# Performance work log

Measured on AMD Instinct MI355X. Metric: run time of the kernel, lower is better.

Reference implementation:

```python
import jax, jax.numpy as jnp
import numpy as np

B, SX, SY, C, M, OUT = 1024, 180, 130, 3, 16, 180
VR_MEAN, VR_STD, EPS = 400.0, 100.0, 1e-5
FLAT = C * SX * SY  # 70200
HID1, HID2 = 2808, OUT


def setup_inputs() -> dict:
    key = jax.random.key(0)
    ks = jax.random.split(key, 16)
    scale = 1.0 / (C * C)
    inp = {
        "x": jax.random.normal(ks[0], (B, SX, SY + 1), dtype=jnp.float32),
        # spectral weights stored as real pairs [in,out,m1,m2,2] like torch view_as_real
        "w1_0": scale * jax.random.uniform(ks[1], (C, C, M, M, 2), dtype=jnp.float32),
        "w2_0": scale * jax.random.uniform(ks[2], (C, C, M, M, 2), dtype=jnp.float32),
        "w1_1": scale * jax.random.uniform(ks[3], (C, C, M, M, 2), dtype=jnp.float32),
        "w2_1": scale * jax.random.uniform(ks[4], (C, C, M, M, 2), dtype=jnp.float32),
        "out1_w1": jax.random.normal(ks[5], (HID1, FLAT), dtype=jnp.float32) * (1.0 / np.sqrt(FLAT)),
        "out1_b1": jnp.zeros((HID1,), dtype=jnp.float32),
        "out1_w2": jax.random.normal(ks[6], (OUT, HID1), dtype=jnp.float32) * (1.0 / np.sqrt(HID1)),
        "out1_b2": jnp.zeros((OUT,), dtype=jnp.float32),
        "reg2_w1": jax.random.normal(ks[7], (OUT, 2 * OUT), dtype=jnp.float32) * (1.0 / np.sqrt(2 * OUT)),
        "reg2_b1": jnp.zeros((OUT,), dtype=jnp.float32),
        "reg2_w2": jax.random.normal(ks[8], (OUT, OUT), dtype=jnp.float32) * (1.0 / np.sqrt(OUT)),
        "reg2_b2": jnp.zeros((OUT,), dtype=jnp.float32),
    }
    return inp


def _cplx(w):
    return w[..., 0] + 1j * w[..., 1]


def _inorm(x):
    # InstanceNorm2d, affine=False: normalize each (b,c) map over spatial dims
    mu = jnp.mean(x, axis=(2, 3), keepdims=True)
    var = jnp.var(x, axis=(2, 3), keepdims=True)
    return (x - mu) * jax.lax.rsqrt(var + EPS)


def _spectral_conv(x, w1, w2):
    # x: [B,C,SX,SY]
    xft = jnp.fft.rfft2(x)  # [B,C,SX,SY//2+1]
    o1 = jnp.einsum('bixy,ioxy->boxy', xft[:, :, :M, :M], _cplx(w1))
    o2 = jnp.einsum('bixy,ioxy->boxy', xft[:, :, -M:, :M], _cplx(w2))
    out_ft = jnp.zeros(xft.shape, dtype=xft.dtype)
    out_ft = out_ft.at[:, :, :M, :M].set(o1)
    out_ft = out_ft.at[:, :, -M:, :M].set(o2)
    return jnp.fft.irfft2(out_ft, s=(SX, SY))


def reference(x, w1_0, w2_0, w1_1, w2_1, out1_w1, out1_b1, out1_w2, out1_b2,
              reg2_w1, reg2_b1, reg2_w2, reg2_b2):
    x0 = x[:, :, -1]                      # [B,180]
    h = x[:, :SX, :-1][..., None]         # [B,180,130,1]
    gx = jnp.linspace(0.0, 1.0, SX, dtype=jnp.float32)[None, :, None, None]
    gy = jnp.linspace(0.0, 1.0, SY, dtype=jnp.float32)[None, None, :, None]
    grid = jnp.concatenate([jnp.broadcast_to(gx, (x.shape[0], SX, SY, 1)),
                            jnp.broadcast_to(gy, (x.shape[0], SX, SY, 1))], axis=-1)
    h = jnp.concatenate([h, grid], axis=-1)          # [B,180,130,3]
    h = jnp.transpose(h, (0, 3, 1, 2))               # [B,3,180,130]
    h = jax.nn.gelu(_inorm(_spectral_conv(_inorm(h), w1_0, w2_0)), approximate=False)
    h = jax.nn.gelu(_inorm(_spectral_conv(_inorm(h), w1_1, w2_1)), approximate=False)
    h = h.reshape(h.shape[0], -1)                    # [B,70200]
    h = jax.nn.relu(h @ out1_w1.T + out1_b1) @ out1_w2.T + out1_b2  # [B,180]
    x0n = (x0 - VR_MEAN) / VR_STD
    # stack pred & normalized residual per output, interleave: [B,180,2] -> [B,360]
    h = jnp.stack([h, x0n], axis=-1).reshape(h.shape[0], -1)
    h = jax.nn.relu(h @ reg2_w1.T + reg2_b1) @ reg2_w2.T + reg2_b2
    return h * VR_STD + VR_MEAN
```

## Files before the change

kernel.cpp:

```cpp
#include <hip/hip_runtime.h>
#include <hip/hip_bf16.h>
#include <math.h>

#ifndef M_PI
#define M_PI 3.14159265358979323846
#endif

#define B_    1024
#define SX    180
#define SY    130
#define NC    3
#define IMG   23400
#define FLATK 70200
#define KPAD  70208
#define HID1  2808
#define NOUT  180
#define XROW  131
#define H1STR 2816
#define KSTEPS 2194
#define KCH8   275
#define NKZ    8

typedef __attribute__((ext_vector_type(8))) short short8;
typedef __attribute__((ext_vector_type(4))) float f32x4;
typedef __attribute__((address_space(3))) unsigned int lds_u32;
typedef __attribute__((address_space(1))) const unsigned int glb_u32;

#define TY_SH   5632
#define TX_SH   12800
#define TXI_SH  13824
#define TIY_SH  6144

__device__ __forceinline__ unsigned short f2bf(float f){
  __hip_bfloat16 h = __float2bfloat16(f);
  return __builtin_bit_cast(unsigned short, h);
}
__device__ __forceinline__ float bf2f(unsigned short u){
  __hip_bfloat16 h = __builtin_bit_cast(__hip_bfloat16, u);
  return __bfloat162float(h);
}
__device__ __forceinline__ void split_bf(float f, unsigned short &hi, unsigned short &lo){
  hi = f2bf(f);
  lo = f2bf(f - bf2f(hi));
}
__device__ __forceinline__ void gl_lds16(const void* g, void* l){
  __builtin_amdgcn_global_load_lds((glb_u32*)g, (lds_u32*)l, 16, 0, 0);
}
__device__ __forceinline__ float gelu_f(float v){
  return 0.5f * v * (1.0f + erff(v * 0.70710678118654752f));
}
__device__ __forceinline__ short8 ld_g8(const unsigned short* p){
  return *(const short8*)p;
}

__global__ void k_tables2(unsigned short* __restrict__ TyH, unsigned short* __restrict__ TyL,
                          unsigned short* __restrict__ TxH, unsigned short* __restrict__ TxL,
                          unsigned short* __restrict__ TxiH, unsigned short* __restrict__ TxiL,
                          unsigned short* __restrict__ TiyH, unsigned short* __restrict__ TiyL){
  int i = blockIdx.x*256 + threadIdx.x;
  unsigned short h, l;
  if (i < TY_SH){
    int m = i/168, y = i%168;
    float v = 0.f;
    if (m < 32 && y < SY){
      int ky = m>>1, ri = m&1;
      double ang = 2.0*M_PI*(double)((ky*y)%SY)/(double)SY;
      v = ri ? (float)(-sin(ang)) : (float)cos(ang);
    }
    split_bf(v,h,l); TyH[i]=h; TyL[i]=l;
  }
  if (i < TX_SH){
    int n = i/200, x = i%200;
    float v = 0.f;
    if (x < SX){
      int kxi = n>>1, ri = n&1;
      int kx = (kxi<16)? kxi : kxi+148;
      double ang = 2.0*M_PI*(double)((kx*x)%SX)/(double)SX;
      v = ri ? (float)sin(ang) : (float)cos(ang);
    }
    split_bf(v,h,l); TxH[i]=h; TxL[i]=l;
  }
  if (i < TXI_SH){
    int x = i/72, k = i%72;
    float v = 0.f;
    if (x < SX && k < 64){
      int kxi = k>>1, ri = k&1;
      int kx = (kxi<16)? kxi : kxi+148;
      double ang = 2.0*M_PI*(double)((kx*x)%SX)/(double)SX;
      v = (float)((ri ? sin(ang) : cos(ang)) / (double)SX);
    }
    split_bf(v,h,l); TxiH[i]=h; TxiL[i]=l;
  }
  if (i < TIY_SH){
    int y = i/40, m = i%40;
    float v = 0.f;
    if (y < SY && m < 32){
      int ky = m>>1, ri = m&1;
      if (m == 0) v = 1.0f/(float)SY;
      else if (m == 1) v = 0.f;
      else {
        double ang = 2.0*M_PI*(double)((ky*y)%SY)/(double)SY;
        v = (float)((ri ? -2.0*sin(ang) : 2.0*cos(ang)) / (double)SY);
      }
    }
    split_bf(v,h,l); TiyH[i]=h; TiyL[i]=l;
  }
}

__global__ __launch_bounds__(256) void k_fwd0(const float* __restrict__ xin,
                                              const unsigned short* __restrict__ TyH,
                                              const unsigned short* __restrict__ TyL,
                                              const unsigned short* __restrict__ TxH,
                                              const unsigned short* __restrict__ TxL,
                                              float* __restrict__ U1,
                                              float* __restrict__ Ug){
  constexpr int DHI = 0;
  constexpr int YTH = 0, YTL = 6400;
  __shared__ unsigned short LB[32256];
  __shared__ float sred[2][4];
  __shared__ float mb[2];
  int t = threadIdx.x, lane = t&63, wv = t>>6, lr = lane&15, lq = lane>>4;
  int bid = blockIdx.x;

  float s = 0.f, ss = 0.f;
  for (int i=t; i<7680; i+=256){
    int row = i/40, c4 = (i - row*40)*4;
    float v[4];
    #pragma unroll
    for (int j=0;j<4;j++){
      int y = c4 + j;
      float val = 0.f;
      if (row < SX && y < SY){
        if (bid < B_)       val = xin[(size_t)bid*(SX*XROW) + row*XROW + y];
        else if (bid == B_) val = (float)row * (1.0f/179.0f);
        else                val = (float)y * (1.0f/129.0f);
      }
      s += val; ss += val*val;
      v[j] = val;
    }
    ushort4 u; u.x=f2bf(v[0]); u.y=f2bf(v[1]); u.z=f2bf(v[2]); u.w=f2bf(v[3]);
    *(ushort4*)&LB[DHI + row*168 + c4] = u;
  }
  for (int o = 32; o >= 1; o >>= 1){ s += __shfl_down(s,o); ss += __shfl_down(ss,o); }
  if (lane == 0){ sred[0][wv] = s; sred[1][wv] = ss; }
  __syncthreads();
  if (t == 0){
    float S = sred[0][0]+sred[0][1]+sred[0][2]+sred[0][3];
    float SS = sred[1][0]+sred[1][1]+sred[1][2]+sred[1][3];
    float mean = S * (1.0f/IMG);
    float var  = SS * (1.0f/IMG) - mean*mean;
    mb[0] = mean; mb[1] = rsqrtf(var + 1e-5f);
  }
  __syncthreads();

  f32x4 acc[2][3] = {};
  #pragma unroll
  for (int ks=0; ks<5; ks++){
    short8 tyh[2], tyl[2];
    #pragma unroll
    for (int mt=0; mt<2; mt++){
      tyh[mt] = ld_g8(&TyH[(mt*16+lr)*168 + ks*32 + lq*8]);
      tyl[mt] = ld_g8(&TyL[(mt*16+lr)*168 + ks*32 + lq*8]);
    }
    #pragma unroll
    for (int j=0; j<3; j++){
      int xr = (wv*3 + j)*16 + lr;
      short8 dh = *(const short8*)&LB[DHI + xr*168 + ks*32 + lq*8];
      #pragma unroll
      for (int mt=0; mt<2; mt++){
        acc[mt][j] = __builtin_amdgcn_mfma_f32_16x16x32_bf16(tyh[mt], dh, acc[mt][j], 0,0,0);
        acc[mt][j] = __builtin_amdgcn_mfma_f32_16x16x32_bf16(tyl[mt], dh, acc[mt][j], 0,0,0);
      }
    }
  }
  __syncthreads();

  {
    float mean = mb[0], istd = mb[1];
    #pragma unroll
    for (int mt=0; mt<2; mt++){
      #pragma unroll
      for (int j=0; j<3; j++){
        int xr = (wv*3 + j)*16 + lr;
        #pragma unroll
        for (int r=0; r<4; r++){
          int m = mt*16 + lq*4 + r;
          float v = acc[mt][j][r];
          if (m == 0) v -= 130.0f*mean;
          v *= istd;
          unsigned short h,l; split_bf(v,h,l);
          LB[YTH + m*200 + xr] = h;
          LB[YTL + m*200 + xr] = l;
        }
      }
    }
  }
  __syncthreads();

  f32x4 acc2[2] = {};
  #pragma unroll
  for (int ks=0; ks<6; ks++){
    short8 txh = ld_g8(&TxH[(wv*16+lr)*200 + ks*32 + lq*8]);
    short8 txl = ld_g8(&TxL[(wv*16+lr)*200 + ks*32 + lq*8]);
    #pragma unroll
    for (int mt=0; mt<2; mt++){
      short8 yh = *(const short8*)&LB[YTH + (mt*16+lr)*200 + ks*32 + lq*8];
      short8 yl = *(const short8*)&LB[YTL + (mt*16+lr)*200 + ks*32 + lq*8];
      acc2[mt] = __builtin_amdgcn_mfma_f32_16x16x32_bf16(yh, txh, acc2[mt], 0,0,0);
      acc2[mt] = __builtin_amdgcn_mfma_f32_16x16x32_bf16(yl, txh, acc2[mt], 0,0,0);
      acc2[mt] = __builtin_amdgcn_mfma_f32_16x16x32_bf16(yh, txl, acc2[mt], 0,0,0);
    }
  }
  float* Ub = (bid < B_) ? (U1 + (size_t)bid*2048) : (Ug + (size_t)(bid - B_)*2048);
  #pragma unroll
  for (int mt=0; mt<2; mt++){
    #pragma unroll
    for (int r=0; r<4; r++){
      int m = mt*16 + lq*4 + r;
      int n = wv*16 + lr;
      Ub[m*64 + n] = acc2[mt][r];
    }
  }
}

__global__ __launch_bounds__(256) void k_mid(const float* __restrict__ U1,
                                             const float* __restrict__ Ug,
                                             const float* __restrict__ w1,
                                             const float* __restrict__ w2,
                                             const unsigned short* __restrict__ TxiH,
                                             const unsigned short* __restrict__ TxiL,
                                             const unsigned short* __restrict__ TiyH,
                                             const unsigned short* __restrict__ TiyL,
                                             const unsigned short* __restrict__ TyH,
                                             const unsigned short* __restrict__ TyL,
                                             const unsigned short* __restrict__ TxH,
                                             const unsigned short* __restrict__ TxL,
                                             float* __restrict__ U2){
  constexpr int ZFH = 0, ZFL = 2304, GH = 4608, GL = 12288;
  constexpr int DAT = 0;
  constexpr int YTH = 0, YTL = 6400;
  __shared__ unsigned short LB[32256];
  __shared__ float sred[2][4];
  __shared__ float mb[2];
  int t = threadIdx.x, lane = t&63, wv = t>>6, lr = lane&15, lq = lane>>4;
  int bid = blockIdx.x, b = bid/3, o = bid - b*3;

  #pragma unroll
  for (int pp=0; pp<2; pp++){
    int p = t + pp*256;
    int kxi = p & 31, ky = p >> 5;
    const float* w = (kxi < 16) ? w1 : w2;
    int kxm = kxi & 15;
    float ar = 0.f, ai = 0.f;
    #pragma unroll
    for (int i=0; i<3; i++){
      const float* Ui = (i==0) ? (U1 + (size_t)b*2048) : (Ug + (size_t)(i-1)*2048);
      float P = Ui[(2*ky  )*64 + 2*kxi  ];
      float Q = Ui[(2*ky  )*64 + 2*kxi+1];
      float R = Ui[(2*ky+1)*64 + 2*kxi  ];
      float S = Ui[(2*ky+1)*64 + 2*kxi+1];
      float zr = P + S, zi = R - Q;
      size_t wo = ((((size_t)i*3 + o)*16 + kxm)*16 + ky)*2;
      float wr = w[wo], wi = w[wo+1];
      ar += zr*wr - zi*wi;
      ai += zr*wi + zi*wr;
    }
    unsigned short hr,lr_, hi,li, hn,ln;
    split_bf(ar,hr,lr_); split_bf(ai,hi,li); split_bf(-ai,hn,ln);
    LB[ZFH + (2*ky  )*72 + 2*kxi  ] = hr;  LB[ZFL + (2*ky  )*72 + 2*kxi  ] = lr_;
    LB[ZFH + (2*ky  )*72 + 2*kxi+1] = hn;  LB[ZFL + (2*ky  )*72 + 2*kxi+1] = ln;
    LB[ZFH + (2*ky+1)*72 + 2*kxi  ] = hi;  LB[ZFL + (2*ky+1)*72 + 2*kxi  ] = li;
    LB[ZFH + (2*ky+1)*72 + 2*kxi+1] = hr;  LB[ZFL + (2*ky+1)*72 + 2*kxi+1] = lr_;
  }
  __syncthreads();

  f32x4 acc1[2][3] = {};
  #pragma unroll
  for (int ks=0; ks<2; ks++){
    short8 zh[2], zl[2];
    #pragma unroll
    for (int mt=0; mt<2; mt++){
      zh[mt] = *(const short8*)&LB[ZFH + (mt*16+lr)*72 + ks*32 + lq*8];
      zl[mt] = *(const short8*)&LB[ZFL + (mt*16+lr)*72 + ks*32 + lq*8];
    }
    #pragma unroll
    for (int j=0; j<3; j++){
      int x = (wv*3 + j)*16 + lr;
      short8 txh = ld_g8(&TxiH[x*72 + ks*32 + lq*8]);
      short8 txl = ld_g8(&TxiL[x*72 + ks*32 + lq*8]);
      #pragma unroll
      for (int mt=0; mt<2; mt++){
        acc1[mt][j] = __builtin_amdgcn_mfma_f32_16x16x32_bf16(zh[mt], txh, acc1[mt][j], 0,0,0);
        acc1[mt][j] = __builtin_amdgcn_mfma_f32_16x16x32_bf16(zl[mt], txh, acc1[mt][j], 0,0,0);
        acc1[mt][j] = __builtin_amdgcn_mfma_f32_16x16x32_bf16(zh[mt], txl, acc1[mt][j], 0,0,0);
      }
    }
  }
  #pragma unroll
  for (int mt=0; mt<2; mt++){
    #pragma unroll
    for (int j=0; j<3; j++){
      int x = (wv*3 + j)*16 + lr;
      #pragma unroll
      for (int r=0; r<4; r++){
        int m = mt*16 + lq*4 + r;
        unsigned short h,l; split_bf(acc1[mt][j][r], h, l);
        LB[GH + x*40 + m] = h;
        LB[GL + x*40 + m] = l;
      }
    }
  }
  __syncthreads();

  f32x4 acc2[3][9] = {};
  #pragma unroll
  for (int i=0; i<3; i++){
    int x = (wv*3 + i)*16 + lr;
    short8 gh = *(const short8*)&LB[GH + x*40 + lq*8];
    short8 gl = *(const short8*)&LB[GL + x*40 + lq*8];
    #pragma unroll
    for (int yt=0; yt<9; yt++){
      short8 tyh = ld_g8(&TiyH[(yt*16+lr)*40 + lq*8]);
      short8 tyl = ld_g8(&TiyL[(yt*16+lr)*40 + lq*8]);
      acc2[i][yt] = __builtin_amdgcn_mfma_f32_16x16x32_bf16(gh, tyh, acc2[i][yt], 0,0,0);
      acc2[i][yt] = __builtin_amdgcn_mfma_f32_16x16x32_bf16(gl, tyh, acc2[i][yt], 0,0,0);
      acc2[i][yt] = __builtin_amdgcn_mfma_f32_16x16x32_bf16(gh, tyl, acc2[i][yt], 0,0,0);
    }
  }

  float s = 0.f, ss = 0.f;
  #pragma unroll
  for (int i=0; i<3; i++){
    int xt = wv*3 + i;
    #pragma unroll
    for (int yt=0; yt<9; yt++){
      #pragma unroll
      for (int r=0; r<4; r++){
        int x = xt*16 + lq*4 + r;
        int y = yt*16 + lr;
        if (x < SX && y < SY){
          float v = acc2[i][yt][r];
          s += v; ss += v*v;
        }
      }
    }
  }
  for (int off = 32; off >= 1; off >>= 1){ s += __shfl_down(s,off); ss += __shfl_down(ss,off); }
  if (lane == 0){ sred[0][wv] = s; sred[1][wv] = ss; }
  __syncthreads();
  if (t == 0){
    float S = sred[0][0]+sred[0][1]+sred[0][2]+sred[0][3];
    float SS = sred[1][0]+sred[1][1]+sred[1][2]+sred[1][3];
    float mean = S * (1.0f/IMG);
    float var  = SS * (1.0f/IMG) - mean*mean;
    mb[0] = mean; mb[1] = rsqrtf(var + 1e-5f);
  }
  __syncthreads();
  float mean1 = mb[0], istd1 = mb[1];

  for (int i=t; i<8064; i+=256)
    *(ushort4*)&LB[DAT + i*4] = make_ushort4(0,0,0,0);
  float s2 = 0.f, ss2 = 0.f;
  #pragma unroll
  for (int i=0; i<3; i++){
    int xt = wv*3 + i;
    #pragma unroll
    for (int yt=0; yt<9; yt++){
      #pragma unroll
      for (int r=0; r<4; r++){
        int x = xt*16 + lq*4 + r;
        int y = yt*16 + lr;
        float d = 0.f;
        if (x < SX && y < SY){
          d = gelu_f((acc2[i][yt][r] - mean1) * istd1);
          s2 += d; ss2 += d*d;
        }
        acc2[i][yt][r] = d;
      }
    }
  }
  for (int off = 32; off >= 1; off >>= 1){ s2 += __shfl_down(s2,off); ss2 += __shfl_down(ss2,off); }
  if (lane == 0){ sred[0][wv] = s2; sred[1][wv] = ss2; }
  __syncthreads();
  if (t == 0){
    float S = sred[0][0]+sred[0][1]+sred[0][2]+sred[0][3];
    float SS = sred[1][0]+sred[1][1]+sred[1][2]+sred[1][3];
    float mean = S * (1.0f/IMG);
    float var  = SS * (1.0f/IMG) - mean*mean;
    mb[0] = mean; mb[1] = rsqrtf(var + 1e-5f);
  }
  __syncthreads();

  #pragma unroll
  for (int i=0; i<3; i++){
    int xt = wv*3 + i;
    #pragma unroll
    for (int yt=0; yt<9; yt++){
      #pragma unroll
      for (int r=0; r<4; r++){
        int x = xt*16 + lq*4 + r;
        int y = yt*16 + lr;
        if (x < SX && y < SY)
          LB[DAT + x*168 + y] = f2bf(acc2[i][yt][r]);
      }
    }
  }
  __syncthreads();

  f32x4 accf[2][3] = {};
  #pragma unroll
  for (int ks=0; ks<5; ks++){
    short8 tyh[2], tyl[2];
    #pragma unroll
    for (int mt=0; mt<2; mt++){
      tyh[mt] = ld_g8(&TyH[(mt*16+lr)*168 + ks*32 + lq*8]);
      tyl[mt] = ld_g8(&TyL[(mt*16+lr)*168 + ks*32 + lq*8]);
    }
    #pragma unroll
    for (int j=0; j<3; j++){
      int xr = (wv*3 + j)*16 + lr;
      short8 dh = *(const short8*)&LB[DAT + xr*168 + ks*32 + lq*8];
      #pragma unroll
      for (int mt=0; mt<2; mt++){
        accf[mt][j] = __builtin_amdgcn_mfma_f32_16x16x32_bf16(tyh[mt], dh, accf[mt][j], 0,0,0);
        accf[mt][j] = __builtin_amdgcn_mfma_f32_16x16x32_bf16(tyl[mt], dh, accf[mt][j], 0,0,0);
      }
    }
  }
  __syncthreads();

  {
    float mean2 = mb[0], istd2 = mb[1];
    #pragma unroll
    for (int mt=0; mt<2; mt++){
      #pragma unroll
      for (int j=0; j<3; j++){
        int xr = (wv*3 + j)*16 + lr;
        #pragma unroll
        for (int r=0; r<4; r++){
          int m = mt*16 + lq*4 + r;
          float v = accf[mt][j][r];
          if (m == 0) v -= 130.0f*mean2;
          v *= istd2;
          unsigned short h,l; split_bf(v,h,l);
          LB[YTH + m*200 + xr] = h;
          LB[YTL + m*200 + xr] = l;
        }
      }
    }
  }
  __syncthreads();

  f32x4 accu[2] = {};
  #pragma unroll
  for (int ks=0; ks<6; ks++){
    short8 txh = ld_g8(&TxH[(wv*16+lr)*200 + ks*32 + lq*8]);
    short8 txl = ld_g8(&TxL[(wv*16+lr)*200 + ks*32 + lq*8]);
    #pragma unroll
    for (int mt=0; mt<2; mt++){
      short8 yh = *(const short8*)&LB[YTH + (mt*16+lr)*200 + ks*32 + lq*8];
      short8 yl = *(const short8*)&LB[YTL + (mt*16+lr)*200 + ks*32 + lq*8];
      accu[mt] = __builtin_amdgcn_mfma_f32_16x16x32_bf16(yh, txh, accu[mt], 0,0,0);
      accu[mt] = __builtin_amdgcn_mfma_f32_16x16x32_bf16(yl, txh, accu[mt], 0,0,0);
      accu[mt] = __builtin_amdgcn_mfma_f32_16x16x32_bf16(yh, txl, accu[mt], 0,0,0);
    }
  }
  float* Ub = U2 + (size_t)bid*2048;
  #pragma unroll
  for (int mt=0; mt<2; mt++){
    #pragma unroll
    for (int r=0; r<4; r++){
      int m = mt*16 + lq*4 + r;
      int n = wv*16 + lr;
      Ub[m*64 + n] = accu[mt][r];
    }
  }
}

__global__ __launch_bounds__(256) void k_inv1(const float* __restrict__ U2,
                                              const float* __restrict__ w1,
                                              const float* __restrict__ w2,
                                              const unsigned short* __restrict__ TxiH,
                                              const unsigned short* __restrict__ TxiL,
                                              const unsigned short* __restrict__ TiyH,
                                              const unsigned short* __restrict__ TiyL,
                                              unsigned short* __restrict__ Abf){
  constexpr int ZFH = 0, ZFL = 2304, GH = 4608, GL = 12288;
  __shared__ unsigned short LB[19968];
  __shared__ float sred[2][4];
  __shared__ float mb[2];
  int t = threadIdx.x, lane = t&63, wv = t>>6, lr = lane&15, lq = lane>>4;
  int bid = blockIdx.x, b = bid/3, o = bid - b*3;

  #pragma unroll
  for (int pp=0; pp<2; pp++){
    int p = t + pp*256;
    int kxi = p & 31, ky = p >> 5;
    const float* w = (kxi < 16) ? w1 : w2;
    int kxm = kxi & 15;
    float ar = 0.f, ai = 0.f;
    #pragma unroll
    for (int i=0; i<3; i++){
      const float* Ui = U2 + ((size_t)b*3 + i)*2048;
      float P = Ui[(2*ky  )*64 + 2*kxi  ];
      float Q = Ui[(2*ky  )*64 + 2*kxi+1];
      float R = Ui[(2*ky+1)*64 + 2*kxi  ];
      float S = Ui[(2*ky+1)*64 + 2*kxi+1];
      float zr = P + S, zi = R - Q;
      size_t wo = ((((size_t)i*3 + o)*16 + kxm)*16 + ky)*2;
      float wr = w[wo], wi = w[wo+1];
      ar += zr*wr - zi*wi;
      ai += zr*wi + zi*wr;
    }
    unsigned short hr,lr_, hi,li, hn,ln;
    split_bf(ar,hr,lr_); split_bf(ai,hi,li); split_bf(-ai,hn,ln);
    LB[ZFH + (2*ky  )*72 + 2*kxi  ] = hr;  LB[ZFL + (2*ky  )*72 + 2*kxi  ] = lr_;
    LB[ZFH + (2*ky  )*72 + 2*kxi+1] = hn;  LB[ZFL + (2*ky  )*72 + 2*kxi+1] = ln;
    LB[ZFH + (2*ky+1)*72 + 2*kxi  ] = hi;  LB[ZFL + (2*ky+1)*72 + 2*kxi  ] = li;
    LB[ZFH + (2*ky+1)*72 + 2*kxi+1] = hr;  LB[ZFL + (2*ky+1)*72 + 2*kxi+1] = lr_;
  }
  __syncthreads();

  f32x4 acc1[2][3] = {};
  #pragma unroll
  for (int ks=0; ks<2; ks++){
    short8 zh[2], zl[2];
    #pragma unroll
    for (int mt=0; mt<2; mt++){
      zh[mt] = *(const short8*)&LB[ZFH + (mt*16+lr)*72 + ks*32 + lq*8];
      zl[mt] = *(const short8*)&LB[ZFL + (mt*16+lr)*72 + ks*32 + lq*8];
    }
    #pragma unroll
    for (int j=0; j<3; j++){
      int x = (wv*3 + j)*16 + lr;
      short8 txh = ld_g8(&TxiH[x*72 + ks*32 + lq*8]);
      short8 txl = ld_g8(&TxiL[x*72 + ks*32 + lq*8]);
      #pragma unroll
      for (int mt=0; mt<2; mt++){
        acc1[mt][j] = __builtin_amdgcn_mfma_f32_16x16x32_bf16(zh[mt], txh, acc1[mt][j], 0,0,0);
        acc1[mt][j] = __builtin_amdgcn_mfma_f32_16x16x32_bf16(zl[mt], txh, acc1[mt][j], 0,0,0);
        acc1[mt][j] = __builtin_amdgcn_mfma_f32_16x16x32_bf16(zh[mt], txl, acc1[mt][j], 0,0,0);
      }
    }
  }
  #pragma unroll
  for (int mt=0; mt<2; mt++){
    #pragma unroll
    for (int j=0; j<3; j++){
      int x = (wv*3 + j)*16 + lr;
      #pragma unroll
      for (int r=0; r<4; r++){
        int m = mt*16 + lq*4 + r;
        unsigned short h,l; split_bf(acc1[mt][j][r], h, l);
        LB[GH + x*40 + m] = h;
        LB[GL + x*40 + m] = l;
      }
    }
  }
  __syncthreads();

  f32x4 acc2[3][9] = {};
  #pragma unroll
  for (int i=0; i<3; i++){
    int x = (wv*3 + i)*16 + lr;
    short8 gh = *(const short8*)&LB[GH + x*40 + lq*8];
    short8 gl = *(const short8*)&LB[GL + x*40 + lq*8];
    #pragma unroll
    for (int yt=0; yt<9; yt++){
      short8 tyh = ld_g8(&TiyH[(yt*16+lr)*40 + lq*8]);
      short8 tyl = ld_g8(&TiyL[(yt*16+lr)*40 + lq*8]);
      acc2[i][yt] = __builtin_amdgcn_mfma_f32_16x16x32_bf16(gh, tyh, acc2[i][yt], 0,0,0);
      acc2[i][yt] = __builtin_amdgcn_mfma_f32_16x16x32_bf16(gl, tyh, acc2[i][yt], 0,0,0);
      acc2[i][yt] = __builtin_amdgcn_mfma_f32_16x16x32_bf16(gh, tyl, acc2[i][yt], 0,0,0);
    }
  }

  float s = 0.f, ss = 0.f;
  #pragma unroll
  for (int i=0; i<3; i++){
    int xt = wv*3 + i;
    #pragma unroll
    for (int yt=0; yt<9; yt++){
      #pragma unroll
      for (int r=0; r<4; r++){
        int x = xt*16 + lq*4 + r;
        int y = yt*16 + lr;
        if (x < SX && y < SY){
          float v = acc2[i][yt][r];
          s += v; ss += v*v;
        }
      }
    }
  }
  for (int off = 32; off >= 1; off >>= 1){ s += __shfl_down(s,off); ss += __shfl_down(ss,off); }
  if (lane == 0){ sred[0][wv] = s; sred[1][wv] = ss; }
  __syncthreads();
  if (t == 0){
    float S = sred[0][0]+sred[0][1]+sred[0][2]+sred[0][3];
    float SS = sred[1][0]+sred[1][1]+sred[1][2]+sred[1][3];
    float mean = S * (1.0f/IMG);
    float var  = SS * (1.0f/IMG) - mean*mean;
    mb[0] = mean; mb[1] = rsqrtf(var + 1e-5f);
  }
  __syncthreads();
  float mean = mb[0], istd = mb[1];

  unsigned short* dst = Abf + (size_t)b*KPAD + (size_t)o*IMG;
  #pragma unroll
  for (int i=0; i<3; i++){
    int xt = wv*3 + i;
    #pragma unroll
    for (int yt=0; yt<9; yt++){
      #pragma unroll
      for (int r=0; r<4; r++){
        int x = xt*16 + lq*4 + r;
        int y = yt*16 + lr;
        if (x < SX && y < SY){
          float v = (acc2[i][yt][r] - mean) * istd;
          dst[x*SY + y] = f2bf(gelu_f(v));
        }
      }
    }
  }
}

__global__ void k_cvt_w(const float* __restrict__ W, unsigned short* __restrict__ Wbf){
  int row = blockIdx.y;
  int gi = blockIdx.x*256 + threadIdx.x;
  if (gi >= KPAD/8) return;
  unsigned short* dst = Wbf + (size_t)row*KPAD + gi*8;
  if (gi*8 >= FLATK){
    *(ushort4*)dst = make_ushort4(0,0,0,0);
    *(ushort4*)(dst+4) = make_ushort4(0,0,0,0);
    return;
  }
  const float4* src = (const float4*)(W + (size_t)row*FLATK + gi*8);
  float4 v0 = src[0], v1 = src[1];
  ushort4 u0, u1;
  u0.x=f2bf(v0.x); u0.y=f2bf(v0.y); u0.z=f2bf(v0.z); u0.w=f2bf(v0.w);
  u1.x=f2bf(v1.x); u1.y=f2bf(v1.y); u1.z=f2bf(v1.z); u1.w=f2bf(v1.w);
  *(ushort4*)dst = u0;
  *(ushort4*)(dst+4) = u1;
}

__global__ void k_padA(unsigned short* __restrict__ Abf){
  int t = blockIdx.x*256 + threadIdx.x;
  if (t >= B_*2) return;
  int b = t >> 1, h = t & 1;
  *(ushort4*)&Abf[(size_t)b*KPAD + FLATK + h*4] = make_ushort4(0,0,0,0);
}

__global__ __launch_bounds__(256) void k_gemm_fast(const unsigned short* __restrict__ Abf,
                                                   const unsigned short* __restrict__ Wbf,
                                                   float* __restrict__ Cpart){
  __shared__ unsigned short As[2][128*32];
  __shared__ unsigned short Bs[2][128*32];
  int t = threadIdx.x;
  int lid = blockIdx.x;
  int xcd = lid & 7, inner = lid >> 3;
  int gq = inner >> 3, bx = inner & 7;
  int g = gq*8 + xcd;
  int by = g >> 3, kz = g & 7;
  int ks0 = kz*KCH8, ks1 = min(ks0 + KCH8, KSTEPS);
  int lane = t & 63, wv = t >> 6;
  int lr = lane & 15, lq = lane >> 4;
  int wr = wv >> 1, wc = wv & 1;
  int srow = t >> 2;
  int scol = ((t & 3) ^ ((srow >> 1) & 3)) * 8;
  const unsigned short* ga0 = Abf + (size_t)(bx*128 + srow)*KPAD + scol;
  const unsigned short* ga1 = ga0 + (size_t)64*KPAD;
  int wrow0 = min(by*128 + srow, HID1-1);
  int wrow1 = min(by*128 + 64 + srow, HID1-1);
  const unsigned short* gb0 = Wbf + (size_t)wrow0*KPAD + scol;
  const unsigned short* gb1 = Wbf + (size_t)wrow1*KPAD + scol;
  int lofs = srow*32 + (t & 3)*8;
  f32x4 acc[4][4] = {};

  {
    size_t gk = (size_t)ks0*32;
    gl_lds16(ga0 + gk, &As[0][lofs]);
    gl_lds16(ga1 + gk, &As[0][2048 + lofs]);
    gl_lds16(gb0 + gk, &Bs[0][lofs]);
    gl_lds16(gb1 + gk, &Bs[0][2048 + lofs]);
  }
  int cur = 0;
  for (int ks = ks0; ks < ks1; ks++){
    if (ks + 1 < ks1){
      size_t gk = (size_t)(ks+1)*32;
      int nb = cur ^ 1;
      gl_lds16(ga0 + gk, &As[nb][lofs]);
      gl_lds16(ga1 + gk, &As[nb][2048 + lofs]);
      gl_lds16(gb0 + gk, &Bs[nb][lofs]);
      gl_lds16(gb1 + gk, &Bs[nb][2048 + lofs]);
      asm volatile("s_waitcnt vmcnt(4)" ::: "memory");
    } else {
      asm volatile("s_waitcnt vmcnt(0)" ::: "memory");
    }
    __builtin_amdgcn_s_barrier();
    short8 a[4], b[4];
    #pragma unroll
    for (int m = 0; m < 4; m++){
      int ra = wr*64 + m*16 + lr;
      a[m] = *(const short8*)&As[cur][ra*32 + (lq ^ ((ra >> 1) & 3))*8];
    }
    #pragma unroll
    for (int n = 0; n < 4; n++){
      int rb = wc*64 + n*16 + lr;
      b[n] = *(const short8*)&Bs[cur][rb*32 + (lq ^ ((rb >> 1) & 3))*8];
    }
    #pragma unroll
    for (int m = 0; m < 4; m++){
      #pragma unroll
      for (int n = 0; n < 4; n++){
        acc[m][n] = __builtin_amdgcn_mfma_f32_16x16x32_bf16(a[m], b[n], acc[m][n], 0, 0, 0);
      }
    }
    __builtin_amdgcn_s_barrier();
    cur ^= 1;
  }
  float* Cp = Cpart + (size_t)kz*B_*H1STR;
  #pragma unroll
  for (int m = 0; m < 4; m++){
    int grow = bx*128 + wr*64 + m*16 + lq*4;
    #pragma unroll
    for (int n = 0; n < 4; n++){
      int gcol = by*128 + wc*64 + n*16 + lr;
      #pragma unroll
      for (int r = 0; r < 4; r++)
        Cp[(size_t)(grow + r)*H1STR + gcol] = acc[m][n][r];
    }
  }
}

__global__ void k_red(const float* __restrict__ Cp, const float* __restrict__ bias,
                      float* __restrict__ h1){
  size_t idx = (size_t)(blockIdx.x*256 + threadIdx.x)*4;
  if (idx >= (size_t)B_*H1STR) return;
  int col = (int)(idx % H1STR);
  float4 acc = make_float4(0.f,0.f,0.f,0.f);
  #pragma unroll
  for (int j = 0; j < NKZ; j++){
    float4 v = *(const float4*)(Cp + (size_t)j*B_*H1STR + idx);
    acc.x += v.x; acc.y += v.y; acc.z += v.z; acc.w += v.w;
  }
  float4 o;
  o.x = fmaxf(acc.x + ((col+0)<HID1 ? bias[col+0] : 0.f), 0.f);
  o.y = fmaxf(acc.y + ((col+1)<HID1 ? bias[col+1] : 0.f), 0.f);
  o.z = fmaxf(acc.z + ((col+2)<HID1 ? bias[col+2] : 0.f), 0.f);
  o.w = fmaxf(acc.w + ((col+3)<HID1 ? bias[col+3] : 0.f), 0.f);
  *(float4*)(h1 + idx) = o;
}

__global__ __launch_bounds__(256) void k_gemm2(const float* __restrict__ h1,
                                               const float* __restrict__ w2,
                                               const float* __restrict__ b2,
                                               float* __restrict__ o1){
  __shared__ float hs[16][68];
  __shared__ float wsm[16][68];
  int t = threadIdx.x;
  int bx = blockIdx.x, by = blockIdx.y;
  int r = t >> 4, c4 = (t & 15) * 4;
  int bi = t >> 4, oi = t & 15;
  float acc = 0.f;
  for (int ks = 0; ks < 44; ks++){
    int gk = ks*64 + c4;
    float4 va = make_float4(0.f,0.f,0.f,0.f);
    if (gk < HID1) va = *(const float4*)&h1[(size_t)(bx*16 + r)*H1STR + gk];
    *(float4*)&hs[r][c4] = va;
    int go = by*16 + r;
    float4 vb = make_float4(0.f,0.f,0.f,0.f);
    if (gk < HID1 && go < NOUT) vb = *(const float4*)&w2[(size_t)go*HID1 + gk];
    *(float4*)&wsm[r][c4] = vb;
    __syncthreads();
    #pragma unroll 8
    for (int k = 0; k < 64; k++) acc += hs[bi][k] * wsm[oi][k];
    __syncthreads();
  }
  int go = by*16 + oi;
  if (go < NOUT) o1[(size_t)(bx*16 + bi)*NOUT + go] = acc + b2[go];
}

__global__ void k_reg2(const float* __restrict__ o1, const float* __restrict__ xin,
                       const float* __restrict__ w1, const float* __restrict__ b1,
                       const float* __restrict__ w2, const float* __restrict__ b2,
                       float* __restrict__ outp){
  __shared__ float s[360];
  __shared__ float tt[180];
  int b = blockIdx.x, t = threadIdx.x;
  if (t < 180){
    s[2*t]   = o1[b*NOUT + t];
    s[2*t+1] = (xin[(size_t)b*SX*XROW + t*XROW + (XROW-1)] - 400.0f) * 0.01f;
  }
  __syncthreads();
  if (t < 180){
    float a = b1[t];
    for (int j = 0; j < 360; j++) a += s[j] * w1[t*360 + j];
    tt[t] = fmaxf(a, 0.0f);
  }
  __syncthreads();
  if (t < 180){
    float a = b2[t];
    for (int j = 0; j < 180; j++) a += tt[j] * w2[t*180 + j];
    outp[b*NOUT + t] = a*100.0f + 400.0f;
  }
}

extern "C" void kernel_launch(void* const* d_in, const int* in_sizes, int n_in,
                              void* d_out, int out_size, void* d_ws, size_t ws_size,
                              hipStream_t stream){
  const float* xin   = (const float*)d_in[0];
  const float* wA0   = (const float*)d_in[1];
  const float* wB0   = (const float*)d_in[2];
  const float* wA1   = (const float*)d_in[3];
  const float* wB1   = (const float*)d_in[4];
  const float* o1w1  = (const float*)d_in[5];
  const float* o1b1  = (const float*)d_in[6];
  const float* o1w2  = (const float*)d_in[7];
  const float* o1b2  = (const float*)d_in[8];
  const float* r2w1  = (const float*)d_in[9];
  const float* r2b1  = (const float*)d_in[10];
  const float* r2w2  = (const float*)d_in[11];
  const float* r2b2  = (const float*)d_in[12];
  float* ws  = (float*)d_ws;
  float* out = (float*)d_out;

  unsigned short* tab = (unsigned short*)ws;
  unsigned short *TyH = tab,            *TyL = tab + TY_SH;
  unsigned short *TxH = TyL + TY_SH,    *TxL = TxH + TX_SH;
  unsigned short *TxiH = TxL + TX_SH,   *TxiL = TxiH + TXI_SH;
  unsigned short *TiyH = TxiL + TXI_SH, *TiyL = TiyH + TIY_SH;

  size_t oU1  = 38400;
  size_t oUg  = oU1  + (size_t)B_*2048;
  size_t oU2  = oUg  + 4096;
  size_t oAbf = oU2  + (size_t)3072*2048;
  size_t oWbf = oAbf + (size_t)B_*KPAD/2;
  size_t oCp  = oWbf + (size_t)HID1*KPAD/2;
  size_t oH1  = oCp  + (size_t)NKZ*B_*H1STR;
  size_t oO1  = oH1  + (size_t)B_*H1STR;

  float *U1 = ws + oU1, *Ug = ws + oUg, *U2 = ws + oU2;
  unsigned short *Abf = (unsigned short*)(ws + oAbf);
  unsigned short *Wbf = (unsigned short*)(ws + oWbf);
  float *Cpart = ws + oCp, *H1 = ws + oH1, *O1 = ws + oO1;

  k_tables2<<<54, 256, 0, stream>>>(TyH, TyL, TxH, TxL, TxiH, TxiL, TiyH, TiyL);

  k_fwd0<<<B_ + 2, 256, 0, stream>>>(xin, TyH, TyL, TxH, TxL, U1, Ug);
  k_mid<<<3072, 256, 0, stream>>>(U1, Ug, wA0, wB0, TxiH, TxiL, TiyH, TiyL,
                                  TyH, TyL, TxH, TxL, U2);
  k_inv1<<<3072, 256, 0, stream>>>(U2, wA1, wB1, TxiH, TxiL, TiyH, TiyL, Abf);

  k_padA<<<8, 256, 0, stream>>>(Abf);
  k_cvt_w<<<dim3(35, HID1), 256, 0, stream>>>(o1w1, Wbf);
  k_gemm_fast<<<1408, 256, 0, stream>>>(Abf, Wbf, Cpart);
  k_red<<<(B_*H1STR/4 + 255)/256, 256, 0, stream>>>(Cpart, o1b1, H1);
  k_gemm2<<<dim3(64, 12), 256, 0, stream>>>(H1, o1w2, o1b2, O1);
  k_reg2<<<B_, 192, 0, stream>>>(O1, xin, r2w1, r2b1, r2w2, r2b2, out);
}
```

Measured before the change: 1.238 ms.

## Fold weight bf16 conversion into spectral kernels and halve GEMM split-K

Converts the large out1_w1 weight matrix to bf16 using extra blocks appended to the three spectral-stage kernels, one third of the rows per kernel, so the memory-bound conversion overlaps with the compute-heavy FFT stages. The A-padding kernel is folded in the same way, which removes two launches. The first GEMM's split-K factor also drops from 8 to 4, halving the partial-sum buffer traffic in the reduction kernel but leaving fewer blocks (704) to fill the GPU. Appended blocks holding LDS allocation may reduce occupancy for the conversion work.

```diff
diff --git a/kernel.cpp b/kernel.cpp
--- a/kernel.cpp
+++ b/kernel.cpp
@@ -18,8 +18,9 @@
 #define XROW  131
 #define H1STR 2816
 #define KSTEPS 2194
-#define KCH8   275
-#define NKZ    8
+#define KCH    549
+#define NKZ    4
+#define WTHIRD 936
 
 typedef __attribute__((ext_vector_type(8))) short short8;
 typedef __attribute__((ext_vector_type(4))) float f32x4;
@@ -51,6 +52,27 @@
 }
 __device__ __forceinline__ short8 ld_g8(const unsigned short* p){
   return *(const short8*)p;
+}
+
+__device__ __forceinline__ void cvt_w_row(const float* __restrict__ W,
+                                          unsigned short* __restrict__ Wbf, int row){
+  int t = threadIdx.x;
+  const float* src = W + (size_t)row*FLATK;
+  unsigned short* dst = Wbf + (size_t)row*KPAD;
+  for (int gi = t; gi < KPAD/8; gi += 256){
+    if (gi*8 >= FLATK){
+      *(ushort4*)(dst + gi*8)     = make_ushort4(0,0,0,0);
+      *(ushort4*)(dst + gi*8 + 4) = make_ushort4(0,0,0,0);
+    } else {
+      float4 v0 = *(const float4*)(src + gi*8);
+      float4 v1 = *(const float4*)(src + gi*8 + 4);
+      ushort4 u0, u1;
+      u0.x=f2bf(v0.x); u0.y=f2bf(v0.y); u0.z=f2bf(v0.z); u0.w=f2bf(v0.w);
+      u1.x=f2bf(v1.x); u1.y=f2bf(v1.y); u1.z=f2bf(v1.z); u1.w=f2bf(v1.w);
+      *(ushort4*)(dst + gi*8)     = u0;
+      *(ushort4*)(dst + gi*8 + 4) = u1;
+    }
+  }
 }
 
 __global__ void k_tables2(unsigned short* __restrict__ TyH, unsigned short* __restrict__ TyL,
@@ -113,14 +135,18 @@
                                               const unsigned short* __restrict__ TxH,
                                               const unsigned short* __restrict__ TxL,
                                               float* __restrict__ U1,
-                                              float* __restrict__ Ug){
+                                              float* __restrict__ Ug,
+                                              const float* __restrict__ Wsrc,
+                                              unsigned short* __restrict__ Wbf){
+  constexpr int MAIN = B_ + 2;
+  int bid = blockIdx.x;
+  if (bid >= MAIN){ cvt_w_row(Wsrc, Wbf, bid - MAIN); return; }
   constexpr int DHI = 0;
   constexpr int YTH = 0, YTL = 6400;
   __shared__ unsigned short LB[32256];
   __shared__ float sred[2][4];
   __shared__ float mb[2];
   int t = threadIdx.x, lane = t&63, wv = t>>6, lr = lane&15, lq = lane>>4;
-  int bid = blockIdx.x;
 
   float s = 0.f, ss = 0.f;
   for (int i=t; i<7680; i+=256){
@@ -235,7 +261,12 @@
                                              const unsigned short* __restrict__ TyL,
                                              const unsigned short* __restrict__ TxH,
                                              const unsigned short* __restrict__ TxL,
-                                             float* __restrict__ U2){
+                                             float* __restrict__ U2,
+                                             const float* __restrict__ Wsrc,
+                                             unsigned short* __restrict__ Wbf){
+  constexpr int MAIN = 3072;
+  int bid = blockIdx.x;
+  if (bid >= MAIN){ cvt_w_row(Wsrc, Wbf, WTHIRD + bid - MAIN); return; }
   constexpr int ZFH = 0, ZFL = 2304, GH = 4608, GL = 12288;
   constexpr int DAT = 0;
   constexpr int YTH = 0, YTL = 6400;
@@ -243,7 +274,7 @@
   __shared__ float sred[2][4];
   __shared__ float mb[2];
   int t = threadIdx.x, lane = t&63, wv = t>>6, lr = lane&15, lq = lane>>4;
-  int bid = blockIdx.x, b = bid/3, o = bid - b*3;
+  int b = bid/3, o = bid - b*3;
 
   #pragma unroll
   for (int pp=0; pp<2; pp++){
@@ -484,13 +515,28 @@
                                               const unsigned short* __restrict__ TxiL,
                                               const unsigned short* __restrict__ TiyH,
                                               const unsigned short* __restrict__ TiyL,
-                                              unsigned short* __restrict__ Abf){
+                                              unsigned short* __restrict__ Abf,
+                                              const float* __restrict__ Wsrc,
+                                              unsigned short* __restrict__ Wbf){
+  constexpr int MAIN = 3072;
+  int bid = blockIdx.x;
+  if (bid >= MAIN){
+    int r = bid - MAIN;
+    if (r < WTHIRD){ cvt_w_row(Wsrc, Wbf, 2*WTHIRD + r); }
+    else {
+      for (int i = threadIdx.x; i < B_*2; i += 256){
+        int b = i >> 1, h = i & 1;
+        *(ushort4*)&Abf[(size_t)b*KPAD + FLATK + h*4] = make_ushort4(0,0,0,0);
+      }
+    }
+    return;
+  }
   constexpr int ZFH = 0, ZFL = 2304, GH = 4608, GL = 12288;
   __shared__ unsigned short LB[19968];
   __shared__ float sred[2][4];
   __shared__ float mb[2];
   int t = threadIdx.x, lane = t&63, wv = t>>6, lr = lane&15, lq = lane>>4;
-  int bid = blockIdx.x, b = bid/3, o = bid - b*3;
+  int b = bid/3, o = bid - b*3;
 
   #pragma unroll
   for (int pp=0; pp<2; pp++){
@@ -624,32 +670,6 @@
   }
 }
 
-__global__ void k_cvt_w(const float* __restrict__ W, unsigned short* __restrict__ Wbf){
-  int row = blockIdx.y;
-  int gi = blockIdx.x*256 + threadIdx.x;
-  if (gi >= KPAD/8) return;
-  unsigned short* dst = Wbf + (size_t)row*KPAD + gi*8;
-  if (gi*8 >= FLATK){
-    *(ushort4*)dst = make_ushort4(0,0,0,0);
-    *(ushort4*)(dst+4) = make_ushort4(0,0,0,0);
-    return;
-  }
-  const float4* src = (const float4*)(W + (size_t)row*FLATK + gi*8);
-  float4 v0 = src[0], v1 = src[1];
-  ushort4 u0, u1;
-  u0.x=f2bf(v0.x); u0.y=f2bf(v0.y); u0.z=f2bf(v0.z); u0.w=f2bf(v0.w);
-  u1.x=f2bf(v1.x); u1.y=f2bf(v1.y); u1.z=f2bf(v1.z); u1.w=f2bf(v1.w);
-  *(ushort4*)dst = u0;
-  *(ushort4*)(dst+4) = u1;
-}
-
-__global__ void k_padA(unsigned short* __restrict__ Abf){
-  int t = blockIdx.x*256 + threadIdx.x;
-  if (t >= B_*2) return;
-  int b = t >> 1, h = t & 1;
-  *(ushort4*)&Abf[(size_t)b*KPAD + FLATK + h*4] = make_ushort4(0,0,0,0);
-}
-
 __global__ __launch_bounds__(256) void k_gemm_fast(const unsigned short* __restrict__ Abf,
                                                    const unsigned short* __restrict__ Wbf,
                                                    float* __restrict__ Cpart){
@@ -660,8 +680,8 @@
   int xcd = lid & 7, inner = lid >> 3;
   int gq = inner >> 3, bx = inner & 7;
   int g = gq*8 + xcd;
-  int by = g >> 3, kz = g & 7;
-  int ks0 = kz*KCH8, ks1 = min(ks0 + KCH8, KSTEPS);
+  int by = g >> 2, kz = g & 3;
+  int ks0 = kz*KCH, ks1 = min(ks0 + KCH, KSTEPS);
   int lane = t & 63, wv = t >> 6;
   int lr = lane & 15, lq = lane >> 4;
   int wr = wv >> 1, wc = wv & 1;
@@ -846,14 +866,13 @@
 
   k_tables2<<<54, 256, 0, stream>>>(TyH, TyL, TxH, TxL, TxiH, TxiL, TiyH, TiyL);
 
-  k_fwd0<<<B_ + 2, 256, 0, stream>>>(xin, TyH, TyL, TxH, TxL, U1, Ug);
-  k_mid<<<3072, 256, 0, stream>>>(U1, Ug, wA0, wB0, TxiH, TxiL, TiyH, TiyL,
-                                  TyH, TyL, TxH, TxL, U2);
-  k_inv1<<<3072, 256, 0, stream>>>(U2, wA1, wB1, TxiH, TxiL, TiyH, TiyL, Abf);
-
-  k_padA<<<8, 256, 0, stream>>>(Abf);
-  k_cvt_w<<<dim3(35, HID1), 256, 0, stream>>>(o1w1, Wbf);
-  k_gemm_fast<<<1408, 256, 0, stream>>>(Abf, Wbf, Cpart);
+  k_fwd0<<<B_ + 2 + WTHIRD, 256, 0, stream>>>(xin, TyH, TyL, TxH, TxL, U1, Ug, o1w1, Wbf);
+  k_mid<<<3072 + WTHIRD, 256, 0, stream>>>(U1, Ug, wA0, wB0, TxiH, TxiL, TiyH, TiyL,
+                                           TyH, TyL, TxH, TxL, U2, o1w1, Wbf);
+  k_inv1<<<3072 + WTHIRD + 1, 256, 0, stream>>>(U2, wA1, wB1, TxiH, TxiL, TiyH, TiyL,
+                                                Abf, o1w1, Wbf);
+
+  k_gemm_fast<<<704, 256, 0, stream>>>(Abf, Wbf, Cpart);
   k_red<<<(B_*H1STR/4 + 255)/256, 256, 0, stream>>>(Cpart, o1b1, H1);
   k_gemm2<<<dim3(64, 12), 256, 0, stream>>>(H1, o1w2, o1b2, O1);
   k_reg2<<<B_, 192, 0, stream>>>(O1, xin, r2w1, r2b1, r2w2, r2b2, out);
```

Result: no change. 1.214 ms (-1.9%).
